# Optimization experiments

Hardware: AMD Instinct MI355X
Metric: run time of the kernel (lower is better)

## Reference

```python
import jax, jax.numpy as jnp
import numpy as np

B, S, HIDDEN = 1, 2048, 2048
NUM_HEADS, MLA_DIM = 16, 128
HEAD_DIM = HIDDEN // NUM_HEADS
ROPE_BASE = 10000.0


def setup_inputs() -> dict:
    key = jax.random.key(0)
    ks = jax.random.split(key, 5)
    sd = 0.02
    hidden_states = jax.random.normal(ks[0], (B, S, HIDDEN), dtype=jnp.float32)
    wq = jax.random.normal(ks[1], (HIDDEN, NUM_HEADS * MLA_DIM), dtype=jnp.float32) * sd
    wk = jax.random.normal(ks[2], (HIDDEN, NUM_HEADS * MLA_DIM), dtype=jnp.float32) * sd
    wv = jax.random.normal(ks[3], (HIDDEN, HIDDEN), dtype=jnp.float32) * sd
    wo = jax.random.normal(ks[4], (HIDDEN, HIDDEN), dtype=jnp.float32) * sd
    # causal additive mask [B, 1, S, S]
    causal = jnp.tril(jnp.ones((S, S), dtype=bool))
    attention_mask = jnp.where(causal, 0.0, -1e9).astype(jnp.float32)[None, None]
    attention_mask = jnp.broadcast_to(attention_mask, (B, 1, S, S))
    return {"hidden_states": hidden_states, "wq": wq, "wk": wk, "wv": wv,
            "wo": wo, "attention_mask": attention_mask}


def _rope_cos_sin(seq_len, dim, dtype):
    inv_freq = 1.0 / (ROPE_BASE ** (jnp.arange(0, dim, 2, dtype=jnp.float32) / dim))
    t = jnp.arange(seq_len, dtype=jnp.float32)
    freqs = jnp.einsum('i,j->ij', t, inv_freq)           # [S, dim/2]
    emb = jnp.concatenate([freqs, freqs], axis=-1)       # [S, dim]
    cos = jnp.cos(emb)[None, :, None, :].astype(dtype)   # [1, S, 1, dim]
    sin = jnp.sin(emb)[None, :, None, :].astype(dtype)
    return cos, sin


def _rotate_half(x):
    x1, x2 = jnp.split(x, 2, axis=-1)
    return jnp.concatenate([-x2, x1], axis=-1)


def reference(hidden_states, wq, wk, wv, wo, attention_mask):
    b, s, _ = hidden_states.shape
    q = (hidden_states @ wq).reshape(b, s, NUM_HEADS, MLA_DIM)
    k = (hidden_states @ wk).reshape(b, s, NUM_HEADS, MLA_DIM)
    v = (hidden_states @ wv).reshape(b, s, NUM_HEADS, HEAD_DIM)
    cos, sin = _rope_cos_sin(s, MLA_DIM, q.dtype)
    q = q * cos + _rotate_half(q) * sin
    k = k * cos + _rotate_half(k) * sin
    scale = 1.0 / np.sqrt(MLA_DIM)
    scores = jnp.einsum('bqhd,bkhd->bhqk', q, k) * scale + attention_mask
    probs = jax.nn.softmax(scores, axis=-1)
    out = jnp.einsum('bhqk,bkhd->bqhd', probs, v).reshape(b, s, HIDDEN)
    return out @ wo
```

## Files before the change

kernel.cpp:

```cpp
#include <hip/hip_runtime.h>
#include <math.h>

namespace {

constexpr int SEQ = 2048;
constexpr int HID = 2048;
constexpr int NH  = 16;
constexpr int DH  = 128;

using f32x4  = __attribute__((ext_vector_type(4))) float;
using short8 = __attribute__((ext_vector_type(8))) short;

__device__ __forceinline__ unsigned short f2bf(float f) {
    unsigned u = __float_as_uint(f);
    u += 0x7FFFu + ((u >> 16) & 1u);
    return (unsigned short)(u >> 16);
}

typedef const __attribute__((address_space(1))) unsigned int GUI;
typedef __attribute__((address_space(3))) unsigned int LUI;
__device__ __forceinline__ void async16(const void* g, void* l) {
    __builtin_amdgcn_global_load_lds((GUI*)g, (LUI*)l, 16, 0, 0);
}

__global__ __launch_bounds__(256)
void cast_bf16(const float* __restrict__ X, unsigned short* __restrict__ Y)
{
    const int i = blockIdx.x * 256 + threadIdx.x;
    const float4 v = reinterpret_cast<const float4*>(X)[i];
    ushort4 o;
    o.x = f2bf(v.x); o.y = f2bf(v.y); o.z = f2bf(v.z); o.w = f2bf(v.w);
    reinterpret_cast<ushort4*>(Y)[i] = o;
}

__global__ __launch_bounds__(256)
void transpose_cast3(const float* __restrict__ w0, const float* __restrict__ w1,
                     const float* __restrict__ w2, unsigned short* __restrict__ WT3)
{
    const int z = blockIdx.z;
    const float* W = (z == 0) ? w0 : (z == 1) ? w1 : w2;
    unsigned short* WT = WT3 + (size_t)z * HID * HID;

    __shared__ float t[32][66];
    const int tx = threadIdx.x & 31, ty = threadIdx.x >> 5;
    const int n0 = blockIdx.x * 64, k0 = blockIdx.y * 32;
    #pragma unroll
    for (int i = 0; i < 4; ++i) {
        const int kr = ty + 8 * i;
        const float2 v = *reinterpret_cast<const float2*>(
            &W[(size_t)(k0 + kr) * HID + n0 + 2 * tx]);
        t[kr][2 * tx]     = v.x;
        t[kr][2 * tx + 1] = v.y;
    }
    __syncthreads();
    #pragma unroll
    for (int i = 0; i < 8; ++i) {
        const int n = ty + 8 * i;
        WT[(size_t)(n0 + n) * HID + k0 + tx] = f2bf(t[tx][n]);
    }
}

__global__ __launch_bounds__(256)
void transpose_cast(const float* __restrict__ W, unsigned short* __restrict__ WT)
{
    __shared__ float t[32][66];
    const int tx = threadIdx.x & 31, ty = threadIdx.x >> 5;
    const int n0 = blockIdx.x * 64, k0 = blockIdx.y * 32;
    #pragma unroll
    for (int i = 0; i < 4; ++i) {
        const int kr = ty + 8 * i;
        const float2 v = *reinterpret_cast<const float2*>(
            &W[(size_t)(k0 + kr) * HID + n0 + 2 * tx]);
        t[kr][2 * tx]     = v.x;
        t[kr][2 * tx + 1] = v.y;
    }
    __syncthreads();
    #pragma unroll
    for (int i = 0; i < 8; ++i) {
        const int n = ty + 8 * i;
        WT[(size_t)(n0 + n) * HID + k0 + tx] = f2bf(t[tx][n]);
    }
}

__global__ __launch_bounds__(256)
void transp_bf16(const unsigned short* __restrict__ X, unsigned short* __restrict__ Y)
{
    __shared__ unsigned short t[32][34];
    const int tx = threadIdx.x & 31, ty = threadIdx.x >> 5;
    const int i0 = blockIdx.y * 32, j0 = blockIdx.x * 32;
    #pragma unroll
    for (int q = 0; q < 4; ++q)
        t[ty + 8 * q][tx] = X[(size_t)(i0 + ty + 8 * q) * HID + j0 + tx];
    __syncthreads();
    #pragma unroll
    for (int q = 0; q < 4; ++q)
        Y[(size_t)(j0 + ty + 8 * q) * HID + i0 + tx] = t[tx][ty + 8 * q];
}

__global__ __launch_bounds__(256)
void gemm_qkv(const unsigned short* __restrict__ A,
              const unsigned short* __restrict__ Bt3,
              unsigned short* __restrict__ Qo,
              unsigned short* __restrict__ Ko,
              unsigned short* __restrict__ Vo)
{
    __shared__ unsigned short As[128 * 32];
    __shared__ unsigned short Bs[128 * 32];

    const int tid  = threadIdx.x;
    const int lane = tid & 63;
    const int w    = tid >> 6;
    const int wr   = w >> 1, wc = w & 1;

    const int b  = blockIdx.x;
    const int sw = (b & 7) * 96 + (b >> 3);
    const int mt = sw & 15, nt = sw >> 4;
    const int m0  = mt * 128;
    const int n0g = nt * 128;
    const int wi  = nt >> 4;
    const int n0  = (nt & 15) * 128;
    unsigned short* C = (wi == 0) ? Qo : (wi == 1) ? Ko : Vo;

    const int srow = lane >> 2;
    const int scol = (lane & 3) * 8;
    const int c0   = w * 2;

    const unsigned short* gA = A   + (size_t)(m0  + c0 * 16 + srow) * HID + scol;
    const unsigned short* gB = Bt3 + (size_t)(n0g + c0 * 16 + srow) * HID + scol;
    unsigned short* lA = &As[c0 * 16 * 32];
    unsigned short* lB = &Bs[c0 * 16 * 32];

    f32x4 acc[4][4] = {};

    for (int k0 = 0; k0 < HID; k0 += 32) {
        __syncthreads();
        async16(gA + k0,            lA);
        async16(gA + 16 * HID + k0, lA + 16 * 32);
        async16(gB + k0,            lB);
        async16(gB + 16 * HID + k0, lB + 16 * 32);
        __syncthreads();

        short8 af[4], bf[4];
        const int kb = (lane >> 4) * 8;
        #pragma unroll
        for (int i = 0; i < 4; ++i) {
            af[i] = *reinterpret_cast<const short8*>(
                &As[(wr * 64 + i * 16 + (lane & 15)) * 32 + kb]);
            bf[i] = *reinterpret_cast<const short8*>(
                &Bs[(wc * 64 + i * 16 + (lane & 15)) * 32 + kb]);
        }
        #pragma unroll
        for (int i = 0; i < 4; ++i)
            #pragma unroll
            for (int j = 0; j < 4; ++j)
                acc[i][j] = __builtin_amdgcn_mfma_f32_16x16x32_bf16(
                    af[i], bf[j], acc[i][j], 0, 0, 0);
    }

    const int cl = lane & 15, rg = (lane >> 4) * 4;
    #pragma unroll
    for (int i = 0; i < 4; ++i)
        #pragma unroll
        for (int j = 0; j < 4; ++j)
            #pragma unroll
            for (int rr = 0; rr < 4; ++rr) {
                const int row = m0 + wr * 64 + i * 16 + rg + rr;
                const int col = n0 + wc * 64 + j * 16 + cl;
                C[(size_t)row * HID + col] = f2bf(acc[i][j][rr]);
            }
}

__global__ __launch_bounds__(256)
void gemm_wo_sk(const unsigned short* __restrict__ A,
                const unsigned short* __restrict__ Bt,
                float* __restrict__ P0, float* __restrict__ P1)
{
    __shared__ unsigned short As[128 * 32];
    __shared__ unsigned short Bs[128 * 32];

    const int tid  = threadIdx.x;
    const int lane = tid & 63;
    const int w    = tid >> 6;
    const int wr   = w >> 1, wc = w & 1;

    const int b     = blockIdx.x;
    const int chunk = b >> 8;
    const int bb    = b & 255;
    const int sw = (bb & 7) * 32 + (bb >> 3);
    const int m0 = (sw >> 4) * 128, n0 = (sw & 15) * 128;
    float* C = chunk ? P1 : P0;
    const int kbase = chunk * 1024;

    const int srow = lane >> 2;
    const int scol = (lane & 3) * 8;
    const int c0   = w * 2;

    const unsigned short* gA = A  + (size_t)(m0 + c0 * 16 + srow) * HID + kbase + scol;
    const unsigned short* gB = Bt + (size_t)(n0 + c0 * 16 + srow) * HID + kbase + scol;
    unsigned short* lA = &As[c0 * 16 * 32];
    unsigned short* lB = &Bs[c0 * 16 * 32];

    f32x4 acc[4][4] = {};

    for (int k0 = 0; k0 < 1024; k0 += 32) {
        __syncthreads();
        async16(gA + k0,            lA);
        async16(gA + 16 * HID + k0, lA + 16 * 32);
        async16(gB + k0,            lB);
        async16(gB + 16 * HID + k0, lB + 16 * 32);
        __syncthreads();

        short8 af[4], bf[4];
        const int kb = (lane >> 4) * 8;
        #pragma unroll
        for (int i = 0; i < 4; ++i) {
            af[i] = *reinterpret_cast<const short8*>(
                &As[(wr * 64 + i * 16 + (lane & 15)) * 32 + kb]);
            bf[i] = *reinterpret_cast<const short8*>(
                &Bs[(wc * 64 + i * 16 + (lane & 15)) * 32 + kb]);
        }
        #pragma unroll
        for (int i = 0; i < 4; ++i)
            #pragma unroll
            for (int j = 0; j < 4; ++j)
                acc[i][j] = __builtin_amdgcn_mfma_f32_16x16x32_bf16(
                    af[i], bf[j], acc[i][j], 0, 0, 0);
    }

    const int cl = lane & 15, rg = (lane >> 4) * 4;
    #pragma unroll
    for (int i = 0; i < 4; ++i)
        #pragma unroll
        for (int j = 0; j < 4; ++j)
            #pragma unroll
            for (int rr = 0; rr < 4; ++rr) {
                const int row = m0 + wr * 64 + i * 16 + rg + rr;
                const int col = n0 + wc * 64 + j * 16 + cl;
                C[(size_t)row * HID + col] = acc[i][j][rr];
            }
}

__global__ __launch_bounds__(256)
void reduce2(const float* __restrict__ P0, const float* __restrict__ P1,
             float* __restrict__ out)
{
    const int i = blockIdx.x * 256 + threadIdx.x;
    const float4 a = reinterpret_cast<const float4*>(P0)[i];
    const float4 b = reinterpret_cast<const float4*>(P1)[i];
    float4 r; r.x = a.x + b.x; r.y = a.y + b.y; r.z = a.z + b.z; r.w = a.w + b.w;
    reinterpret_cast<float4*>(out)[i] = r;
}

__global__ __launch_bounds__(256)
void rope_qk(unsigned short* __restrict__ Q, unsigned short* __restrict__ K)
{
    const int idx = blockIdx.x * 256 + threadIdx.x;
    const int d = idx & 63;
    const int h = (idx >> 6) & (NH - 1);
    const int s = idx >> 10;

    const float invf = exp2f(-(float)d * (13.287712379549449f / 64.0f));
    float sn, c;
    sincosf((float)s * invf, &sn, &c);

    const float SC = 0.08838834764831845f;
    const size_t base = (size_t)s * HID + h * DH + d;

    const float a0 = __uint_as_float((unsigned)Q[base]      << 16);
    const float a1 = __uint_as_float((unsigned)Q[base + 64] << 16);
    Q[base]      = f2bf((a0 * c - a1 * sn) * SC);
    Q[base + 64] = f2bf((a1 * c + a0 * sn) * SC);
    const float b0 = __uint_as_float((unsigned)K[base]      << 16);
    const float b1 = __uint_as_float((unsigned)K[base + 64] << 16);
    K[base]      = f2bf(b0 * c - b1 * sn);
    K[base + 64] = f2bf(b1 * c + b0 * sn);
}

__global__ __launch_bounds__(256)
void attn_mfma(const unsigned short* __restrict__ Q,
               const unsigned short* __restrict__ K,
               const unsigned short* __restrict__ Vt,
               unsigned short* __restrict__ AO)
{
    __shared__ unsigned short Ks[2][64 * 128];
    __shared__ unsigned short Vs[2][128 * 64];
    __shared__ unsigned short Ps[4][16 * 72];

    const int tid  = threadIdx.x;
    const int lane = tid & 63;
    const int w    = tid >> 6;

    const int b  = blockIdx.x;
    const int i_ = b & 31;
    const int h  = b >> 5;
    const int qb = (b < 256) ? i_ : 31 - i_;
    const int q0 = qb * 64;

    const int cl = lane & 15;
    const int lg = lane >> 4;
    const int rg = lg * 4;

    short8 aq[4];
    const unsigned short* qrow = Q + (size_t)(q0 + w * 16 + cl) * HID + h * DH;
    #pragma unroll
    for (int c = 0; c < 4; ++c)
        aq[c] = *reinterpret_cast<const short8*>(qrow + c * 32 + lg * 8);

    f32x4 o[8] = {};
    float m[4] = {-INFINITY, -INFINITY, -INFINITY, -INFINITY};
    float l[4] = {};

    auto stage = [&](int t, int buf) {
        const int k0 = t * 64;
        #pragma unroll
        for (int i = 0; i < 4; ++i) {
            const int rb = i * 16 + w * 4;
            const int r  = rb + lg;
            const int gs = cl ^ (r & 7);
            async16(K + (size_t)(k0 + r) * HID + h * DH + gs * 8,
                    &Ks[buf][rb * 128]);
        }
        #pragma unroll
        for (int i = 0; i < 4; ++i) {
            const int rb = i * 32 + w * 8;
            const int r  = rb + (lane >> 3);
            const int gs = (lane & 7) ^ (r & 7);
            async16(Vt + (size_t)(h * DH + r) * SEQ + k0 + gs * 8,
                    &Vs[buf][rb * 64]);
        }
    };

    const int nt = qb + 1;
    stage(0, 0);

    for (int t = 0; t < nt; ++t) {
        const int cur = t & 1;
        __syncthreads();
        if (t + 1 < nt) stage(t + 1, cur ^ 1);

        f32x4 s4[4] = {};
        #pragma unroll
        for (int jk = 0; jk < 4; ++jk) {
            #pragma unroll
            for (int c = 0; c < 4; ++c) {
                const int row  = jk * 16 + cl;
                const int slot = (c * 4 + lg) ^ (row & 7);
                const short8 bk = *reinterpret_cast<const short8*>(
                    &Ks[cur][row * 128 + slot * 8]);
                s4[jk] = __builtin_amdgcn_mfma_f32_16x16x32_bf16(
                    aq[c], bk, s4[jk], 0, 0, 0);
            }
        }

        if (t == nt - 1) {
            #pragma unroll
            for (int jk = 0; jk < 4; ++jk)
                #pragma unroll
                for (int r = 0; r < 4; ++r)
                    if (jk * 16 + cl > w * 16 + rg + r)
                        s4[jk][r] = -INFINITY;
        }

        float corr[4], rs[4];
        #pragma unroll
        for (int r = 0; r < 4; ++r) {
            float mx = fmaxf(fmaxf(s4[0][r], s4[1][r]),
                             fmaxf(s4[2][r], s4[3][r]));
            #pragma unroll
            for (int off = 1; off < 16; off <<= 1)
                mx = fmaxf(mx, __shfl_xor(mx, off, 64));
            const float mn = fmaxf(m[r], mx);
            corr[r] = __expf(m[r] - mn);
            m[r] = mn;
            rs[r] = 0.0f;
        }
        #pragma unroll
        for (int jk = 0; jk < 4; ++jk)
            #pragma unroll
            for (int r = 0; r < 4; ++r) {
                const float p = __expf(s4[jk][r] - m[r]);
                Ps[w][(rg + r) * 72 + jk * 16 + cl] = f2bf(p);
                rs[r] += p;
            }
        #pragma unroll
        for (int r = 0; r < 4; ++r) {
            #pragma unroll
            for (int off = 1; off < 16; off <<= 1)
                rs[r] += __shfl_xor(rs[r], off, 64);
            l[r] = l[r] * corr[r] + rs[r];
        }
        #pragma unroll
        for (int jd = 0; jd < 8; ++jd)
            #pragma unroll
            for (int r = 0; r < 4; ++r)
                o[jd][r] *= corr[r];

        #pragma unroll
        for (int c = 0; c < 2; ++c) {
            const short8 pa = *reinterpret_cast<const short8*>(
                &Ps[w][cl * 72 + c * 32 + lg * 8]);
            #pragma unroll
            for (int jd = 0; jd < 8; ++jd) {
                const int row  = jd * 16 + cl;
                const int slot = (c * 4 + lg) ^ (row & 7);
                const short8 bv = *reinterpret_cast<const short8*>(
                    &Vs[cur][row * 64 + slot * 8]);
                o[jd] = __builtin_amdgcn_mfma_f32_16x16x32_bf16(
                    pa, bv, o[jd], 0, 0, 0);
            }
        }
    }

    #pragma unroll
    for (int r = 0; r < 4; ++r) {
        const float inv = 1.0f / l[r];
        unsigned short* orow = AO + (size_t)(q0 + w * 16 + rg + r) * HID + h * DH;
        #pragma unroll
        for (int jd = 0; jd < 8; ++jd)
            orow[jd * 16 + cl] = f2bf(o[jd][r] * inv);
    }
}

}

extern "C" void kernel_launch(void* const* d_in, const int* in_sizes, int n_in,
                              void* d_out, int out_size, void* d_ws, size_t ws_size,
                              hipStream_t stream)
{
    (void)in_sizes; (void)n_in; (void)out_size; (void)ws_size;

    const float* hs = (const float*)d_in[0];
    const float* wq = (const float*)d_in[1];
    const float* wk = (const float*)d_in[2];
    const float* wv = (const float*)d_in[3];
    const float* wo = (const float*)d_in[4];
    float* out = (float*)d_out;

    const size_t NE = (size_t)SEQ * HID;
    unsigned short* hsb = (unsigned short*)d_ws;
    unsigned short* Qb  = hsb + NE;
    unsigned short* Kb  = Qb + NE;
    unsigned short* Vb  = Kb + NE;
    unsigned short* WT3 = Vb + NE;
    unsigned short* AOb = WT3 + NE;
    unsigned short* WTo = WT3;
    unsigned short* Vt  = hsb;
    float* P0 = (float*)hsb;
    float* P1 = (float*)Kb;

    cast_bf16<<<(NE / 4) / 256, 256, 0, stream>>>(hs, hsb);

    transpose_cast3<<<dim3(HID / 64, HID / 32, 3), 256, 0, stream>>>(wq, wk, wv, WT3);

    gemm_qkv<<<768, 256, 0, stream>>>(hsb, WT3, Qb, Kb, Vb);

    rope_qk<<<(SEQ * NH * 64) / 256, 256, 0, stream>>>(Qb, Kb);

    transp_bf16<<<dim3(HID / 32, HID / 32), 256, 0, stream>>>(Vb, Vt);

    attn_mfma<<<512, 256, 0, stream>>>(Qb, Kb, Vt, AOb);

    transpose_cast<<<dim3(HID / 64, HID / 32), 256, 0, stream>>>(wo, WTo);
    gemm_wo_sk<<<512, 256, 0, stream>>>(AOb, WTo, P0, P1);
    reduce2<<<(int)(NE / 4 / 256), 256, 0, stream>>>(P0, P1, out);
}
```

Baseline: 313.1 us.

## Split attention KV range across blocks with combine pass; deepen GEMM K tiles

The causal attention kernel becomes a split-KV scheme. Each block handles 128 query rows with 8 warps over at most 12 KV tiles, and long query blocks are split into partial results. A new combine kernel merges those partials using the saved max and sum values. This balances work across the 480 blocks, but it drops the double buffering of K/V and adds extra global traffic for the partials. Both GEMMs also move to 64-wide K tiles, which halves the number of sync iterations at the cost of more LDS per block.

```diff
diff --git a/kernel.cpp b/kernel.cpp
--- a/kernel.cpp
+++ b/kernel.cpp
@@ -11,6 +11,8 @@
 using f32x4  = __attribute__((ext_vector_type(4))) float;
 using short8 = __attribute__((ext_vector_type(8))) short;
 
+__device__ __forceinline__ float bflo(unsigned u) { return __uint_as_float(u << 16); }
+__device__ __forceinline__ float bfhi(unsigned u) { return __uint_as_float(u & 0xFFFF0000u); }
 __device__ __forceinline__ unsigned short f2bf(float f) {
     unsigned u = __float_as_uint(f);
     u += 0x7FFFu + ((u >> 16) & 1u);
@@ -104,8 +106,8 @@
               unsigned short* __restrict__ Ko,
               unsigned short* __restrict__ Vo)
 {
-    __shared__ unsigned short As[128 * 32];
-    __shared__ unsigned short Bs[128 * 32];
+    __shared__ unsigned short As[128 * 64];
+    __shared__ unsigned short Bs[128 * 64];
 
     const int tid  = threadIdx.x;
     const int lane = tid & 63;
@@ -121,43 +123,43 @@
     const int n0  = (nt & 15) * 128;
     unsigned short* C = (wi == 0) ? Qo : (wi == 1) ? Ko : Vo;
 
-    const int srow = lane >> 2;
-    const int scol = (lane & 3) * 8;
-    const int c0   = w * 2;
-
-    const unsigned short* gA = A   + (size_t)(m0  + c0 * 16 + srow) * HID + scol;
-    const unsigned short* gB = Bt3 + (size_t)(n0g + c0 * 16 + srow) * HID + scol;
-    unsigned short* lA = &As[c0 * 16 * 32];
-    unsigned short* lB = &Bs[c0 * 16 * 32];
+    const int srow = lane >> 3;
+    const int sunit = lane & 7;
+    const int cl = lane & 15, lg = lane >> 4;
 
     f32x4 acc[4][4] = {};
 
-    for (int k0 = 0; k0 < HID; k0 += 32) {
+    for (int k0 = 0; k0 < HID; k0 += 64) {
         __syncthreads();
-        async16(gA + k0,            lA);
-        async16(gA + 16 * HID + k0, lA + 16 * 32);
-        async16(gB + k0,            lB);
-        async16(gB + 16 * HID + k0, lB + 16 * 32);
+        #pragma unroll
+        for (int i = 0; i < 4; ++i) {
+            const int rb = (w * 4 + i) * 8;
+            const int r  = rb + srow;
+            async16(A   + (size_t)(m0  + r) * HID + k0 + sunit * 8, &As[rb * 64]);
+            async16(Bt3 + (size_t)(n0g + r) * HID + k0 + sunit * 8, &Bs[rb * 64]);
+        }
         __syncthreads();
 
-        short8 af[4], bf[4];
-        const int kb = (lane >> 4) * 8;
-        #pragma unroll
-        for (int i = 0; i < 4; ++i) {
-            af[i] = *reinterpret_cast<const short8*>(
-                &As[(wr * 64 + i * 16 + (lane & 15)) * 32 + kb]);
-            bf[i] = *reinterpret_cast<const short8*>(
-                &Bs[(wc * 64 + i * 16 + (lane & 15)) * 32 + kb]);
-        }
-        #pragma unroll
-        for (int i = 0; i < 4; ++i)
-            #pragma unroll
-            for (int j = 0; j < 4; ++j)
-                acc[i][j] = __builtin_amdgcn_mfma_f32_16x16x32_bf16(
-                    af[i], bf[j], acc[i][j], 0, 0, 0);
-    }
-
-    const int cl = lane & 15, rg = (lane >> 4) * 4;
+        #pragma unroll
+        for (int ks = 0; ks < 2; ++ks) {
+            short8 af[4], bf[4];
+            #pragma unroll
+            for (int i = 0; i < 4; ++i) {
+                af[i] = *reinterpret_cast<const short8*>(
+                    &As[(wr * 64 + i * 16 + cl) * 64 + ks * 32 + lg * 8]);
+                bf[i] = *reinterpret_cast<const short8*>(
+                    &Bs[(wc * 64 + i * 16 + cl) * 64 + ks * 32 + lg * 8]);
+            }
+            #pragma unroll
+            for (int i = 0; i < 4; ++i)
+                #pragma unroll
+                for (int j = 0; j < 4; ++j)
+                    acc[i][j] = __builtin_amdgcn_mfma_f32_16x16x32_bf16(
+                        af[i], bf[j], acc[i][j], 0, 0, 0);
+        }
+    }
+
+    const int rg = lg * 4;
     #pragma unroll
     for (int i = 0; i < 4; ++i)
         #pragma unroll
@@ -175,8 +177,8 @@
                 const unsigned short* __restrict__ Bt,
                 float* __restrict__ P0, float* __restrict__ P1)
 {
-    __shared__ unsigned short As[128 * 32];
-    __shared__ unsigned short Bs[128 * 32];
+    __shared__ unsigned short As[128 * 64];
+    __shared__ unsigned short Bs[128 * 64];
 
     const int tid  = threadIdx.x;
     const int lane = tid & 63;
@@ -191,43 +193,43 @@
     float* C = chunk ? P1 : P0;
     const int kbase = chunk * 1024;
 
-    const int srow = lane >> 2;
-    const int scol = (lane & 3) * 8;
-    const int c0   = w * 2;
-
-    const unsigned short* gA = A  + (size_t)(m0 + c0 * 16 + srow) * HID + kbase + scol;
-    const unsigned short* gB = Bt + (size_t)(n0 + c0 * 16 + srow) * HID + kbase + scol;
-    unsigned short* lA = &As[c0 * 16 * 32];
-    unsigned short* lB = &Bs[c0 * 16 * 32];
+    const int srow = lane >> 3;
+    const int sunit = lane & 7;
+    const int cl = lane & 15, lg = lane >> 4;
 
     f32x4 acc[4][4] = {};
 
-    for (int k0 = 0; k0 < 1024; k0 += 32) {
+    for (int k0 = 0; k0 < 1024; k0 += 64) {
         __syncthreads();
-        async16(gA + k0,            lA);
-        async16(gA + 16 * HID + k0, lA + 16 * 32);
-        async16(gB + k0,            lB);
-        async16(gB + 16 * HID + k0, lB + 16 * 32);
+        #pragma unroll
+        for (int i = 0; i < 4; ++i) {
+            const int rb = (w * 4 + i) * 8;
+            const int r  = rb + srow;
+            async16(A  + (size_t)(m0 + r) * HID + kbase + k0 + sunit * 8, &As[rb * 64]);
+            async16(Bt + (size_t)(n0 + r) * HID + kbase + k0 + sunit * 8, &Bs[rb * 64]);
+        }
         __syncthreads();
 
-        short8 af[4], bf[4];
-        const int kb = (lane >> 4) * 8;
-        #pragma unroll
-        for (int i = 0; i < 4; ++i) {
-            af[i] = *reinterpret_cast<const short8*>(
-                &As[(wr * 64 + i * 16 + (lane & 15)) * 32 + kb]);
-            bf[i] = *reinterpret_cast<const short8*>(
-                &Bs[(wc * 64 + i * 16 + (lane & 15)) * 32 + kb]);
-        }
-        #pragma unroll
-        for (int i = 0; i < 4; ++i)
-            #pragma unroll
-            for (int j = 0; j < 4; ++j)
-                acc[i][j] = __builtin_amdgcn_mfma_f32_16x16x32_bf16(
-                    af[i], bf[j], acc[i][j], 0, 0, 0);
-    }
-
-    const int cl = lane & 15, rg = (lane >> 4) * 4;
+        #pragma unroll
+        for (int ks = 0; ks < 2; ++ks) {
+            short8 af[4], bf[4];
+            #pragma unroll
+            for (int i = 0; i < 4; ++i) {
+                af[i] = *reinterpret_cast<const short8*>(
+                    &As[(wr * 64 + i * 16 + cl) * 64 + ks * 32 + lg * 8]);
+                bf[i] = *reinterpret_cast<const short8*>(
+                    &Bs[(wc * 64 + i * 16 + cl) * 64 + ks * 32 + lg * 8]);
+            }
+            #pragma unroll
+            for (int i = 0; i < 4; ++i)
+                #pragma unroll
+                for (int j = 0; j < 4; ++j)
+                    acc[i][j] = __builtin_amdgcn_mfma_f32_16x16x32_bf16(
+                        af[i], bf[j], acc[i][j], 0, 0, 0);
+        }
+    }
+
+    const int rg = lg * 4;
     #pragma unroll
     for (int i = 0; i < 4; ++i)
         #pragma unroll
@@ -276,25 +278,36 @@
     K[base + 64] = f2bf(b1 * c + b0 * sn);
 }
 
-__global__ __launch_bounds__(256)
-void attn_mfma(const unsigned short* __restrict__ Q,
+__global__ __launch_bounds__(512, 4)
+void attn_part(const unsigned short* __restrict__ Q,
                const unsigned short* __restrict__ K,
                const unsigned short* __restrict__ Vt,
+               unsigned short* __restrict__ Opart,
+               float2* __restrict__ ML,
                unsigned short* __restrict__ AO)
 {
-    __shared__ unsigned short Ks[2][64 * 128];
-    __shared__ unsigned short Vs[2][128 * 64];
-    __shared__ unsigned short Ps[4][16 * 72];
+    __shared__ unsigned short Ks[64 * 128];
+    __shared__ unsigned short Vs[128 * 64];
+    __shared__ unsigned short Ps[8][16 * 72];
 
     const int tid  = threadIdx.x;
     const int lane = tid & 63;
     const int w    = tid >> 6;
 
-    const int b  = blockIdx.x;
-    const int i_ = b & 31;
-    const int h  = b >> 5;
-    const int qb = (b < 256) ? i_ : 31 - i_;
-    const int q0 = qb * 64;
+    const int h = blockIdx.x / 30;
+    int c = blockIdx.x - h * 30;
+    int qb = 0;
+    while (true) {
+        const int cnt = (qb + 6) / 6;
+        if (c < cnt) break;
+        c -= cnt; ++qb;
+    }
+    const int cnt = (qb + 6) / 6;
+    const int q0 = qb * 128;
+    const int t0 = c * 12;
+    const int t1 = min(2 * (qb + 1), t0 + 12);
+    const bool direct = (cnt == 1);
+    const int pidx = h * 24 + ((qb < 12) ? (qb - 6) * 2 : 12 + (qb - 12) * 3) + c;
 
     const int cl = lane & 15;
     const int lg = lane >> 4;
@@ -303,61 +316,55 @@
     short8 aq[4];
     const unsigned short* qrow = Q + (size_t)(q0 + w * 16 + cl) * HID + h * DH;
     #pragma unroll
-    for (int c = 0; c < 4; ++c)
-        aq[c] = *reinterpret_cast<const short8*>(qrow + c * 32 + lg * 8);
+    for (int cc = 0; cc < 4; ++cc)
+        aq[cc] = *reinterpret_cast<const short8*>(qrow + cc * 32 + lg * 8);
 
     f32x4 o[8] = {};
     float m[4] = {-INFINITY, -INFINITY, -INFINITY, -INFINITY};
     float l[4] = {};
 
-    auto stage = [&](int t, int buf) {
+    for (int t = t0; t < t1; ++t) {
         const int k0 = t * 64;
-        #pragma unroll
-        for (int i = 0; i < 4; ++i) {
-            const int rb = i * 16 + w * 4;
-            const int r  = rb + lg;
+
+        __syncthreads();
+        #pragma unroll
+        for (int i = 0; i < 2; ++i) {
+            const int rb = (w * 2 + i) * 4;
+            const int r  = rb + (lane >> 4);
             const int gs = cl ^ (r & 7);
-            async16(K + (size_t)(k0 + r) * HID + h * DH + gs * 8,
-                    &Ks[buf][rb * 128]);
-        }
-        #pragma unroll
-        for (int i = 0; i < 4; ++i) {
-            const int rb = i * 32 + w * 8;
+            async16(K + (size_t)(k0 + r) * HID + h * DH + gs * 8, &Ks[rb * 128]);
+        }
+        #pragma unroll
+        for (int i = 0; i < 2; ++i) {
+            const int rb = (w * 2 + i) * 8;
             const int r  = rb + (lane >> 3);
             const int gs = (lane & 7) ^ (r & 7);
-            async16(Vt + (size_t)(h * DH + r) * SEQ + k0 + gs * 8,
-                    &Vs[buf][rb * 64]);
-        }
-    };
-
-    const int nt = qb + 1;
-    stage(0, 0);
-
-    for (int t = 0; t < nt; ++t) {
-        const int cur = t & 1;
+            async16(Vt + (size_t)(h * DH + r) * SEQ + k0 + gs * 8, &Vs[rb * 64]);
+        }
         __syncthreads();
-        if (t + 1 < nt) stage(t + 1, cur ^ 1);
 
         f32x4 s4[4] = {};
+        __builtin_amdgcn_s_setprio(1);
         #pragma unroll
         for (int jk = 0; jk < 4; ++jk) {
             #pragma unroll
-            for (int c = 0; c < 4; ++c) {
+            for (int cc = 0; cc < 4; ++cc) {
                 const int row  = jk * 16 + cl;
-                const int slot = (c * 4 + lg) ^ (row & 7);
+                const int slot = (cc * 4 + lg) ^ (row & 7);
                 const short8 bk = *reinterpret_cast<const short8*>(
-                    &Ks[cur][row * 128 + slot * 8]);
+                    &Ks[row * 128 + slot * 8]);
                 s4[jk] = __builtin_amdgcn_mfma_f32_16x16x32_bf16(
-                    aq[c], bk, s4[jk], 0, 0, 0);
-            }
-        }
-
-        if (t == nt - 1) {
+                    aq[cc], bk, s4[jk], 0, 0, 0);
+            }
+        }
+        __builtin_amdgcn_s_setprio(0);
+
+        if (t >= 2 * qb) {
             #pragma unroll
             for (int jk = 0; jk < 4; ++jk)
                 #pragma unroll
                 for (int r = 0; r < 4; ++r)
-                    if (jk * 16 + cl > w * 16 + rg + r)
+                    if (k0 + jk * 16 + cl > q0 + w * 16 + rg + r)
                         s4[jk][r] = -INFINITY;
         }
 
@@ -395,30 +402,90 @@
             for (int r = 0; r < 4; ++r)
                 o[jd][r] *= corr[r];
 
-        #pragma unroll
-        for (int c = 0; c < 2; ++c) {
+        __builtin_amdgcn_s_setprio(1);
+        #pragma unroll
+        for (int cc = 0; cc < 2; ++cc) {
             const short8 pa = *reinterpret_cast<const short8*>(
-                &Ps[w][cl * 72 + c * 32 + lg * 8]);
+                &Ps[w][cl * 72 + cc * 32 + lg * 8]);
             #pragma unroll
             for (int jd = 0; jd < 8; ++jd) {
                 const int row  = jd * 16 + cl;
-                const int slot = (c * 4 + lg) ^ (row & 7);
+                const int slot = (cc * 4 + lg) ^ (row & 7);
                 const short8 bv = *reinterpret_cast<const short8*>(
-                    &Vs[cur][row * 64 + slot * 8]);
+                    &Vs[row * 64 + slot * 8]);
                 o[jd] = __builtin_amdgcn_mfma_f32_16x16x32_bf16(
                     pa, bv, o[jd], 0, 0, 0);
             }
         }
-    }
-
-    #pragma unroll
-    for (int r = 0; r < 4; ++r) {
-        const float inv = 1.0f / l[r];
-        unsigned short* orow = AO + (size_t)(q0 + w * 16 + rg + r) * HID + h * DH;
-        #pragma unroll
-        for (int jd = 0; jd < 8; ++jd)
-            orow[jd * 16 + cl] = f2bf(o[jd][r] * inv);
-    }
+        __builtin_amdgcn_s_setprio(0);
+    }
+
+    if (direct) {
+        #pragma unroll
+        for (int r = 0; r < 4; ++r) {
+            const float inv = 1.0f / l[r];
+            unsigned short* orow =
+                AO + (size_t)(q0 + w * 16 + rg + r) * HID + h * DH;
+            #pragma unroll
+            for (int jd = 0; jd < 8; ++jd)
+                orow[jd * 16 + cl] = f2bf(o[jd][r] * inv);
+        }
+    } else {
+        #pragma unroll
+        for (int r = 0; r < 4; ++r) {
+            const int row = w * 16 + rg + r;
+            if (cl == 0)
+                ML[(size_t)pidx * 128 + row] = make_float2(m[r], l[r]);
+            unsigned short* orow = Opart + ((size_t)pidx * 128 + row) * DH;
+            #pragma unroll
+            for (int jd = 0; jd < 8; ++jd)
+                orow[jd * 16 + cl] = f2bf(o[jd][r]);
+        }
+    }
+}
+
+__global__ __launch_bounds__(256)
+void attn_combine(const unsigned short* __restrict__ Opart,
+                  const float2* __restrict__ ML,
+                  unsigned short* __restrict__ AO)
+{
+    int t = blockIdx.x * 256 + threadIdx.x;
+    const int dp  = t & 63;  t >>= 6;
+    const int row = t & 127; t >>= 7;
+    const int qq  = t % 10;
+    const int h   = t / 10;
+    const int qb  = 6 + qq;
+
+    const int cnt  = (qb < 12) ? 2 : 3;
+    const int base = h * 24 + ((qb < 12) ? (qb - 6) * 2 : 12 + (qb - 12) * 3);
+
+    float mc[3], lc[3];
+    unsigned uc[3];
+    #pragma unroll
+    for (int cc = 0; cc < 3; ++cc) {
+        if (cc < cnt) {
+            const int p = base + cc;
+            const float2 ml = ML[(size_t)p * 128 + row];
+            mc[cc] = ml.x; lc[cc] = ml.y;
+            uc[cc] = reinterpret_cast<const unsigned*>(
+                Opart)[((size_t)p * 128 + row) * 64 + dp];
+        } else { mc[cc] = -INFINITY; lc[cc] = 0.0f; uc[cc] = 0; }
+    }
+
+    float M = fmaxf(mc[0], fmaxf(mc[1], mc[2]));
+    float o0 = 0.0f, o1 = 0.0f, L = 0.0f;
+    #pragma unroll
+    for (int cc = 0; cc < 3; ++cc) {
+        const float e = __expf(mc[cc] - M);
+        o0 += bflo(uc[cc]) * e;
+        o1 += bfhi(uc[cc]) * e;
+        L  += lc[cc] * e;
+    }
+
+    const float inv = 1.0f / L;
+    const unsigned out = (unsigned)f2bf(o0 * inv) | ((unsigned)f2bf(o1 * inv) << 16);
+    const int qrow = qb * 128 + row;
+    reinterpret_cast<unsigned*>(AO)[(size_t)qrow * (HID / 2) + h * (DH / 2) + dp] = out;
 }
 
 }
@@ -442,7 +509,9 @@
     unsigned short* Kb  = Qb + NE;
     unsigned short* Vb  = Kb + NE;
     unsigned short* WT3 = Vb + NE;
-    unsigned short* AOb = WT3 + NE;
+    unsigned short* Opart = WT3;
+    float2* MLp = (float2*)(WT3 + (size_t)384 * 128 * 128);
+    unsigned short* AOb = WT3 + 2 * NE;
     unsigned short* WTo = WT3;
     unsigned short* Vt  = hsb;
     float* P0 = (float*)hsb;
@@ -458,7 +527,8 @@
 
     transp_bf16<<<dim3(HID / 32, HID / 32), 256, 0, stream>>>(Vb, Vt);
 
-    attn_mfma<<<512, 256, 0, stream>>>(Qb, Kb, Vt, AOb);
+    attn_part<<<480, 512, 0, stream>>>(Qb, Kb, Vt, Opart, MLp, AOb);
+    attn_combine<<<(16 * 10 * 128 * 64) / 256, 256, 0, stream>>>(Opart, MLp, AOb);
 
     transpose_cast<<<dim3(HID / 64, HID / 32), 256, 0, stream>>>(wo, WTo);
     gemm_wo_sk<<<512, 256, 0, stream>>>(AOb, WTo, P0, P1);
```

After: 345.8 us. +10.4%, slower.
